# Kernel optimization log

Measured on AMD Instinct MI355X. Metric: run time of the kernel, lower is better.

Reference implementation:

```python
import jax, jax.numpy as jnp
import numpy as np

GROUPS = 8
HEADS = 8
EPS = 1e-5


def group_norm(x, w, b, groups=GROUPS, eps=EPS):
    # x: [B, C, D, H, W]
    B, C, D, H, W = x.shape
    xg = x.reshape(B, groups, C // groups, D, H, W)
    mu = xg.mean(axis=(2, 3, 4, 5), keepdims=True)
    var = xg.var(axis=(2, 3, 4, 5), keepdims=True)
    xn = ((xg - mu) / jnp.sqrt(var + eps)).reshape(B, C, D, H, W)
    return xn * w[None, :, None, None, None] + b[None, :, None, None, None]


def conv1x1(x, w, b):
    # 1x1x1 Conv3d == channel-mixing GEMM. w: [Cout, Cin], x: [B, Cin, D, H, W]
    y = jnp.einsum('oc,bcdhw->bodhw', w, x)
    return y + b[None, :, None, None, None]


def setup_inputs() -> dict:
    key = jax.random.key(0)
    ks = jax.random.split(key, 8)
    C, CTX = 512, 512
    B, D, H, W = 1, 16, 16, 16
    x = jax.random.normal(ks[0], (B, C, D, H, W), dtype=jnp.float32)
    context = jax.random.normal(ks[1], (B, CTX, D, H, W), dtype=jnp.float32)
    return {
        'x': x,
        'context': context,
        'norm_w': jnp.ones((C,), jnp.float32),
        'norm_b': jnp.zeros((C,), jnp.float32),
        'normc_w': jnp.ones((CTX,), jnp.float32),
        'normc_b': jnp.zeros((CTX,), jnp.float32),
        'q_w': jax.random.normal(ks[2], (C, C), jnp.float32) * 0.02,
        'q_b': jnp.zeros((C,), jnp.float32),
        'kv_w': jax.random.normal(ks[3], (2 * C, CTX), jnp.float32) * 0.02,
        'kv_b': jnp.zeros((2 * C,), jnp.float32),
        'proj_w': jax.random.normal(ks[4], (C, C), jnp.float32) * 0.02,
        'proj_b': jnp.zeros((C,), jnp.float32),
    }


def _split_heads(t, heads):
    # [B, (h c), D, H, W] -> [B, h, S, c] with S = D*H*W
    B, C, D, H, W = t.shape
    return t.reshape(B, heads, C // heads, D * H * W).transpose(0, 1, 3, 2)


def reference(x, context, norm_w, norm_b, normc_w, normc_b,
              q_w, q_b, kv_w, kv_b, proj_w, proj_b):
    B, C, D, H, W = x.shape
    h = group_norm(x, norm_w, norm_b)
    c = group_norm(context, normc_w, normc_b)
    q = conv1x1(h, q_w, q_b)
    kv = conv1x1(c, kv_w, kv_b)
    k, v = jnp.split(kv, 2, axis=1)
    q = _split_heads(q, HEADS)   # [B, h, S, c]
    k = _split_heads(k, HEADS)
    v = _split_heads(v, HEADS)
    scale = (C // HEADS) ** (-0.5)
    logits = jnp.einsum('bhqc,bhkc->bhqk', q, k) * scale
    attn = jax.nn.softmax(logits, axis=-1)
    out = jnp.einsum('bhqk,bhkc->bhqc', attn, v)
    # [B, h, S, c] -> [B, (h c), D, H, W]
    out = out.transpose(0, 1, 3, 2).reshape(B, C, D, H, W)
    out = conv1x1(out, proj_w, proj_b)
    return x + out
```

## Files before the change

kernel.cpp:

```cpp
#include <hip/hip_runtime.h>

typedef unsigned short u16;
typedef unsigned int u32;
typedef float f32x4 __attribute__((ext_vector_type(4)));
typedef __bf16 bf16x8 __attribute__((ext_vector_type(8)));
typedef u32 u32x4 __attribute__((ext_vector_type(4)));

#define LOG2E 1.44269504088896340736f

static __device__ __forceinline__ u16 f2bf(float f){ u32 u=__builtin_bit_cast(u32,f); u32 r=u+0x7fffu+((u>>16)&1u); return (u16)(r>>16); }
static __device__ __forceinline__ u32 pk2(float a,float b){ return (u32)f2bf(a)|((u32)f2bf(b)<<16); }
static __device__ __forceinline__ float fexp2(float x){
#if __has_builtin(__builtin_amdgcn_exp2f)
  return __builtin_amdgcn_exp2f(x);
#else
  float r; asm volatile("v_exp_f32 %0, %1" : "=v"(r) : "v"(x)); return r;
#endif
}
static __device__ __forceinline__ f32x4 mfma16(u32x4 a,u32x4 b,f32x4 c){
  return __builtin_amdgcn_mfma_f32_16x16x32_bf16(__builtin_bit_cast(bf16x8,a),__builtin_bit_cast(bf16x8,b),c,0,0,0);
}
static __device__ __forceinline__ u32x4 ldfrag(const u32* p){
  uint2 a=*(const uint2*)p; uint2 b=*(const uint2*)(p+2);
  u32x4 r; r.x=a.x; r.y=a.y; r.z=b.x; r.w=b.y; return r;
}
static __device__ __forceinline__ void stlds(u32* d, uint4 v){
  *(uint2*)d = make_uint2(v.x,v.y); *(uint2*)(d+2) = make_uint2(v.z,v.w);
}
static __device__ __forceinline__ uint4 pack8(float4 a,float4 b){
  uint4 o; o.x=pk2(a.x,a.y); o.y=pk2(a.z,a.w); o.z=pk2(b.x,b.y); o.w=pk2(b.z,b.w); return o;
}

__global__ __launch_bounds__(256) void k_stats(const float* __restrict__ x, const float* __restrict__ c,
                                               float* __restrict__ stats){
  const int g=blockIdx.x>>3, slice=blockIdx.x&7;
  const float* src=(g<8?x:c)+(size_t)(g&7)*262144+(size_t)slice*32768;
  const float4* p=(const float4*)src;
  const int t=threadIdx.x;
  float s1=0.f,s2=0.f;
  for(int i=0;i<32;i++){
    float4 v=p[t+i*256];
    s1+=v.x+v.y+v.z+v.w;
    s2+=v.x*v.x+v.y*v.y+v.z*v.z+v.w*v.w;
  }
  #pragma unroll
  for(int m=1;m<64;m<<=1){ s1+=__shfl_xor(s1,m,64); s2+=__shfl_xor(s2,m,64); }
  __shared__ float r1[4],r2[4];
  const int lane=t&63,w=t>>6;
  if(lane==0){ r1[w]=s1; r2[w]=s2; }
  __syncthreads();
  if(t==0){
    atomicAdd(&stats[2*g],   r1[0]+r1[1]+r1[2]+r1[3]);
    atomicAdd(&stats[2*g+1], r2[0]+r2[1]+r2[2]+r2[3]);
  }
}

__global__ __launch_bounds__(256) void k_prep(const float* __restrict__ qw,const float* __restrict__ qb,
    const float* __restrict__ kvw,const float* __restrict__ kvb,
    const float* __restrict__ nw,const float* __restrict__ nb,
    const float* __restrict__ ncw,const float* __restrict__ ncb,
    const float* __restrict__ pb,const float* __restrict__ stats,
    u16* __restrict__ Wall,float* __restrict__ biasAll){
  const int lane=threadIdx.x&63, w=threadIdx.x>>6;
  const int r=blockIdx.x*4+w;
  if(r>=1536){ if(lane==0) biasAll[r]=pb[r-1536]; return; }
  const bool isq = r<512;
  const float* Wsrc = isq ? qw+(size_t)r*512 : kvw+(size_t)(r-512)*512;
  const float* anw = isq ? nw : ncw;
  const float* anb = isq ? nb : ncb;
  const int gbase = isq ? 0 : 8;
  const float bin = isq ? qb[r] : kvb[r-512];
  const int ci0=lane*8;
  float4 wa=*(const float4*)(Wsrc+ci0);
  float4 wb=*(const float4*)(Wsrc+ci0+4);
  float wf[8]={wa.x,wa.y,wa.z,wa.w,wb.x,wb.y,wb.z,wb.w};
  float bp=0.f; u16 hb[8];
  #pragma unroll
  for(int j=0;j<8;j++){
    int ci=ci0+j;
    int g=gbase+(ci>>6);
    float mean=stats[2*g]*(1.f/262144.f);
    float var =stats[2*g+1]*(1.f/262144.f)-mean*mean;
    float rstd=rsqrtf(var+1e-5f);
    float alv=anw[ci]*rstd;
    float bev=anb[ci]-mean*alv;
    bp+=wf[j]*bev;
    hb[j]=f2bf(wf[j]*alv);
  }
  uint4 ov;
  ov.x=(u32)hb[0]|((u32)hb[1]<<16);
  ov.y=(u32)hb[2]|((u32)hb[3]<<16);
  ov.z=(u32)hb[4]|((u32)hb[5]<<16);
  ov.w=(u32)hb[6]|((u32)hb[7]<<16);
  *(uint4*)(Wall+(size_t)r*512+ci0)=ov;
  #pragma unroll
  for(int m=1;m<64;m<<=1) bp+=__shfl_xor(bp,m,64);
  if(lane==0) biasAll[r]=bin+bp;
}

template<int AMODE,int BMODE,int SMODE,int ZM>
__global__ __launch_bounds__(256) void k_gemm(const void* __restrict__ Av,const void* __restrict__ Av2,
    const void* __restrict__ Bv,const float* __restrict__ biasAll,const float* __restrict__ residf,
    void* __restrict__ out1,void* __restrict__ out2,float scale1,float scale2){
  __shared__ __align__(16) u32 As[2][64*18];
  __shared__ __align__(16) u32 Bs[2][128*18];
  const int t=threadIdx.x, lane=t&63, w=t>>6;
  const int wm=w&1, wn=w>>1, quad=lane>>4, l15=lane&15;
  const int m0=blockIdx.y*64, n0=blockIdx.x*128;
  const int z = ZM ? blockIdx.z : 0;
  const void* Aptr = (ZM && z) ? Av2 : Av;
  const u16* Bu = (const u16*)Bv + (BMODE==0 ? (size_t)z*512*512 : 0);
  const float* Bf = (const float*)Bv;
  const float* bias = biasAll + (ZM ? z*512 : 0);
  void* outv = (ZM && z) ? out2 : out1;
  const float scale = (ZM && z) ? scale2 : scale1;
  const int arow=t>>2, akc=(t&3)*8;
  const int cl=t>>3, s8=(t&7)*8;

  uint4 ra; float4 raf0, raf1;
  uint4 rb0, rb1; float4 rbf0, rbf1, rbf2, rbf3;

  auto loadAB=[&](int kk){
    if(AMODE==0){
      const u16* A=(const u16*)Aptr;
      ra=*(const uint4*)(A+(size_t)(m0+arow)*512+kk+akc);
    }else if(AMODE==1){
      const float* A=(const float*)Aptr;
      raf0=*(const float4*)(A+(size_t)(kk+cl)*4096+m0+s8);
      raf1=*(const float4*)(A+(size_t)(kk+cl)*4096+m0+s8+4);
    }else{
      const float* A=(const float*)Aptr;
      raf0=*(const float4*)(A+(size_t)(m0+arow)*512+kk+akc);
      raf1=*(const float4*)(A+(size_t)(m0+arow)*512+kk+akc+4);
    }
    if(BMODE==2){
      rbf0=*(const float4*)(Bf+(size_t)(kk+cl)*4096+n0+s8);
      rbf1=*(const float4*)(Bf+(size_t)(kk+cl)*4096+n0+s8+4);
      rbf2=*(const float4*)(Bf+(size_t)(kk+cl)*4096+n0+64+s8);
      rbf3=*(const float4*)(Bf+(size_t)(kk+cl)*4096+n0+64+s8+4);
    }else if(BMODE==1){
      rb0=*(const uint4*)(Bu+((size_t)((kk>>6)*4096+n0+arow))*64+(kk&63)+akc);
      rb1=*(const uint4*)(Bu+((size_t)((kk>>6)*4096+n0+64+arow))*64+(kk&63)+akc);
    }else{
      rb0=*(const uint4*)(Bu+(size_t)(n0+arow)*512+kk+akc);
      rb1=*(const uint4*)(Bu+(size_t)(n0+64+arow)*512+kk+akc);
    }
  };
  auto writeAB=[&](u32* Asb,u32* Bsb){
    if(AMODE==0){ stlds(&Asb[arow*18+(akc>>1)],ra); }
    else if(AMODE==1){
      float f[8]={raf0.x,raf0.y,raf0.z,raf0.w,raf1.x,raf1.y,raf1.z,raf1.w};
      u16* As16=(u16*)Asb;
      #pragma unroll
      for(int j=0;j<8;j++) As16[(s8+j)*36+cl]=f2bf(f[j]);
    }else{
      stlds(&Asb[arow*18+(akc>>1)],pack8(raf0,raf1));
    }
    if(BMODE==2){
      u16* Bs16=(u16*)Bsb;
      float f[8]={rbf0.x,rbf0.y,rbf0.z,rbf0.w,rbf1.x,rbf1.y,rbf1.z,rbf1.w};
      float g[8]={rbf2.x,rbf2.y,rbf2.z,rbf2.w,rbf3.x,rbf3.y,rbf3.z,rbf3.w};
      #pragma unroll
      for(int j=0;j<8;j++){
        Bs16[(s8+j)*36+cl]=f2bf(f[j]);
        Bs16[(64+s8+j)*36+cl]=f2bf(g[j]);
      }
    }else{
      stlds(&Bsb[arow*18+(akc>>1)],rb0);
      stlds(&Bsb[(64+arow)*18+(akc>>1)],rb1);
    }
  };

  f32x4 acc[2][4];
  #pragma unroll
  for(int i=0;i<2;i++)
    #pragma unroll
    for(int j=0;j<4;j++){ acc[i][j].x=0.f; acc[i][j].y=0.f; acc[i][j].z=0.f; acc[i][j].w=0.f; }

  auto compute=[&](const u32* Asb,const u32* Bsb){
    const u32* Ab=Asb+(wm*32+l15)*18+quad*4;
    const u32* Bb=Bsb+(wn*64+l15)*18+quad*4;
    u32x4 af[2], bfr[4];
    #pragma unroll
    for(int mt=0;mt<2;mt++) af[mt]=ldfrag(Ab+mt*288);
    #pragma unroll
    for(int nt=0;nt<4;nt++) bfr[nt]=ldfrag(Bb+nt*288);
    #pragma unroll
    for(int mt=0;mt<2;mt++)
      #pragma unroll
      for(int nt=0;nt<4;nt++) acc[mt][nt]=mfma16(af[mt],bfr[nt],acc[mt][nt]);
  };

  loadAB(0); writeAB(As[0],Bs[0]);
  __syncthreads();
  for(int kk=0;kk<512;kk+=64){
    loadAB(kk+32);
    compute(As[0],Bs[0]);
    writeAB(As[1],Bs[1]);
    __syncthreads();
    const bool n2=(kk+64)<512;
    if(n2) loadAB(kk+64);
    compute(As[1],Bs[1]);
    if(n2){ writeAB(As[0],Bs[0]); __syncthreads(); }
  }
  #pragma unroll
  for(int mt=0;mt<2;mt++)
    #pragma unroll
    for(int nt=0;nt<4;nt++){
      const int n = n0 + wn*64 + nt*16 + l15;
      if(SMODE==0){
        u16* out=(u16*)outv;
        const float bn = bias[n];
        const size_t base = ((size_t)((n>>6)*4096))*64 + (size_t)(n&63);
        #pragma unroll
        for(int r=0;r<4;r++){
          int m = m0 + wm*32 + mt*16 + quad*4 + r;
          out[base + (size_t)m*64] = f2bf((acc[mt][nt][r]+bn)*scale);
        }
      } else if(SMODE==1){
        u16* out=(u16*)outv;
        #pragma unroll
        for(int r=0;r<4;r++){
          int m = m0 + wm*32 + mt*16 + quad*4 + r;
          out[(size_t)m*4096+n] = f2bf(acc[mt][nt][r] + bias[m]);
        }
      } else {
        float* out=(float*)outv;
        #pragma unroll
        for(int r=0;r<4;r++){
          int m = m0 + wm*32 + mt*16 + quad*4 + r;
          out[(size_t)m*4096+n] = acc[mt][nt][r] + bias[m] + residf[(size_t)m*4096+n];
        }
      }
    }
}

__global__ __launch_bounds__(256) void k_attn(const u16* __restrict__ Qh,const u16* __restrict__ Kh,
                                              const u16* __restrict__ Vp,u16* __restrict__ Oh){
  __shared__ __align__(16) u32 Qs[64*34];
  __shared__ __align__(16) u32 Ks[2][64*34];
  __shared__ __align__(16) u32 Vs[2][64*34];
  __shared__ __align__(16) u32 Ps[4][16*34];
  const int t=threadIdx.x, lane=t&63, w=t>>6, quad=lane>>4, l15=lane&15;
  const int h=blockIdx.y, s0=blockIdx.x*64;
  const int srow=t>>2, sc=(t&3)*16;
  const u16* Kg = Kh + ((size_t)(h*4096+srow))*64 + sc;
  const u16* Vg = Vp + (size_t)(h*64+srow)*4096 + sc;
  { const u16* p = Qh + ((size_t)(h*4096+s0+srow))*64 + sc;
    stlds(&Qs[srow*34+(sc>>1)],   *(const uint4*)p);
    stlds(&Qs[srow*34+(sc>>1)+4], *(const uint4*)(p+8));
    stlds(&Ks[0][srow*34+(sc>>1)],   *(const uint4*)Kg);
    stlds(&Ks[0][srow*34+(sc>>1)+4], *(const uint4*)(Kg+8));
    stlds(&Vs[0][srow*34+(sc>>1)],   *(const uint4*)Vg);
    stlds(&Vs[0][srow*34+(sc>>1)+4], *(const uint4*)(Vg+8)); }
  __syncthreads();
  u32x4 qf[2];
  #pragma unroll
  for(int ks=0;ks<2;ks++) qf[ks]=ldfrag(&Qs[(w*16+l15)*34+ks*16+quad*4]);
  float lrun[4]; f32x4 oacc[4];
  #pragma unroll
  for(int r=0;r<4;r++) lrun[r]=0.f;
  #pragma unroll
  for(int nt=0;nt<4;nt++){ oacc[nt].x=0.f; oacc[nt].y=0.f; oacc[nt].z=0.f; oacc[nt].w=0.f; }

  u16* Pw=(u16*)Ps[w]+(quad*4)*68+l15;
  const u32* Pb=Ps[w]+l15*34+quad*4;

  auto halfstep=[&](const u32* Kc,const u32* Vc,u32* Kn,u32* Vn,int t0,bool pf){
    uint4 pk0,pk1,pv0,pv1;
    if(pf){
      const u16* kp=Kg+(size_t)(t0+64)*64;
      pk0=*(const uint4*)kp; pk1=*(const uint4*)(kp+8);
      const u16* vp=Vg+(t0+64);
      pv0=*(const uint4*)vp; pv1=*(const uint4*)(vp+8);
    }
    f32x4 sv[4];
    const u32* Kb=Kc+l15*34+quad*4;
    #pragma unroll
    for(int nt=0;nt<4;nt++){
      f32x4 zz; zz.x=0.f; zz.y=0.f; zz.z=0.f; zz.w=0.f;
      u32x4 k0=ldfrag(Kb+nt*544);
      u32x4 k1=ldfrag(Kb+nt*544+16);
      zz=mfma16(qf[0],k0,zz);
      sv[nt]=mfma16(qf[1],k1,zz);
    }
    #pragma unroll
    for(int nt=0;nt<4;nt++)
      #pragma unroll
      for(int r=0;r<4;r++){
        float p=fexp2(sv[nt][r]);
        sv[nt][r]=p;
        Pw[r*68+nt*16]=(u16)(__builtin_bit_cast(u32,p)>>16);
      }
    #pragma unroll
    for(int r=0;r<4;r++) lrun[r]+=(sv[0][r]+sv[1][r])+(sv[2][r]+sv[3][r]);
    const u32* Vb=Vc+l15*34+quad*4;
    #pragma unroll
    for(int ks=0;ks<2;ks++){
      u32x4 pfr=ldfrag(Pb+ks*16);
      #pragma unroll
      for(int nt=0;nt<4;nt++){
        u32x4 vf=ldfrag(Vb+nt*544+ks*16);
        oacc[nt]=mfma16(pfr,vf,oacc[nt]);
      }
    }
    if(pf){
      u32* Knw=Kn+srow*34+(sc>>1);
      u32* Vnw=Vn+srow*34+(sc>>1);
      stlds(Knw,pk0); stlds(Knw+4,pk1);
      stlds(Vnw,pv0); stlds(Vnw+4,pv1);
      __syncthreads();
    }
  };

  for(int t0=0;t0<4096;t0+=128){
    halfstep(Ks[0],Vs[0],Ks[1],Vs[1],t0,true);
    halfstep(Ks[1],Vs[1],Ks[0],Vs[0],t0+64,(t0+128)<4096);
  }

  #pragma unroll
  for(int r=0;r<4;r++){
    float l=lrun[r];
    #pragma unroll
    for(int m=1;m<16;m<<=1) l+=__shfl_xor(l,m,64);
    float inv=1.f/l;
    #pragma unroll
    for(int nt=0;nt<4;nt++) oacc[nt][r]*=inv;
  }
  #pragma unroll
  for(int nt=0;nt<4;nt++)
    #pragma unroll
    for(int r=0;r<4;r++)
      Oh[((size_t)(h*4096+s0+w*16+quad*4+r))*64 + nt*16 + l15]=f2bf(oacc[nt][r]);
}

extern "C" void kernel_launch(void* const* d_in, const int* in_sizes, int n_in,
                              void* d_out, int out_size, void* d_ws, size_t ws_size,
                              hipStream_t stream){
  (void)in_sizes; (void)n_in; (void)out_size; (void)ws_size;
  const float* x  =(const float*)d_in[0];
  const float* ctx=(const float*)d_in[1];
  const float* nw =(const float*)d_in[2];
  const float* nb =(const float*)d_in[3];
  const float* ncw=(const float*)d_in[4];
  const float* ncb=(const float*)d_in[5];
  const float* qw =(const float*)d_in[6];
  const float* qb =(const float*)d_in[7];
  const float* kvw=(const float*)d_in[8];
  const float* kvb=(const float*)d_in[9];
  const float* pw =(const float*)d_in[10];
  const float* pb =(const float*)d_in[11];
  float* out=(float*)d_out;
  char* ws=(char*)d_ws;
  float* stats  =(float*)ws;
  float* biasAll=(float*)(ws+256);
  u16* Wall=(u16*)(ws+16384);
  u16* Qh  =(u16*)(ws+1589248);
  u16* Kh  =(u16*)(ws+5783552);
  u16* Vp  =(u16*)(ws+9977856);
  u16* Oh  =(u16*)(ws+14172160);

  (void)hipMemsetAsync(stats,0,128,stream);
  k_stats<<<dim3(128),dim3(256),0,stream>>>(x,ctx,stats);
  k_prep<<<dim3(512),dim3(256),0,stream>>>(qw,qb,kvw,kvb,nw,nb,ncw,ncb,pb,stats,Wall,biasAll);
  k_gemm<1,0,0,1><<<dim3(4,64,2),dim3(256),0,stream>>>(x, ctx, Wall, biasAll, nullptr, Qh, Kh, 0.125f*LOG2E, 1.f);
  k_gemm<0,2,1,0><<<dim3(32,8),dim3(256),0,stream>>>(Wall+(size_t)1024*512, nullptr, ctx, biasAll+1024, nullptr, Vp, nullptr, 1.f, 1.f);
  k_attn<<<dim3(64,8),dim3(256),0,stream>>>(Qh,Kh,Vp,Oh);
  k_gemm<2,1,2,0><<<dim3(32,8),dim3(256),0,stream>>>(pw, nullptr, Oh, biasAll+1536, x, out, nullptr, 1.f, 1.f);
}
```

Baseline: 207.1 us.

## Split attention KV range across two wave groups and keep P in registers

The attention kernel now runs 512 threads per block. Two halves of four waves each process disjoint halves of the key/value sequence, and their partial outputs and row sums are merged through shared memory at the end. The S tile is computed transposed with 16x16x16 bf16 MFMAs, so the exponentiated probabilities can feed the PV MFMA directly from registers, which removes the per-wave P round-trip through LDS. This doubles parallelism for a grid of only 512 blocks. The cost is smaller MFMA shapes, an extra reduction step, and higher LDS and register pressure per block.

Result: faster. 189.7 us (-8.4%).

```diff
diff --git a/kernel.cpp b/kernel.cpp
--- a/kernel.cpp
+++ b/kernel.cpp
@@ -5,6 +5,8 @@
 typedef float f32x4 __attribute__((ext_vector_type(4)));
 typedef __bf16 bf16x8 __attribute__((ext_vector_type(8)));
 typedef u32 u32x4 __attribute__((ext_vector_type(4)));
+typedef u32 u32x2 __attribute__((ext_vector_type(2)));
+typedef short s16x4 __attribute__((ext_vector_type(4)));
 
 #define LOG2E 1.44269504088896340736f
 
@@ -20,9 +22,21 @@
 static __device__ __forceinline__ f32x4 mfma16(u32x4 a,u32x4 b,f32x4 c){
   return __builtin_amdgcn_mfma_f32_16x16x32_bf16(__builtin_bit_cast(bf16x8,a),__builtin_bit_cast(bf16x8,b),c,0,0,0);
 }
+#if __has_builtin(__builtin_amdgcn_mfma_f32_16x16x16bf16_1k)
+static __device__ __forceinline__ f32x4 mfma1k(s16x4 a,s16x4 b,f32x4 c){
+  return __builtin_amdgcn_mfma_f32_16x16x16bf16_1k(a,b,c,0,0,0);
+}
+#else
+static __device__ __forceinline__ f32x4 mfma1k(s16x4 a,s16x4 b,f32x4 c){
+  f32x4 d; asm("v_mfma_f32_16x16x16_bf16 %0, %1, %2, %3":"=v"(d):"v"(a),"v"(b),"v"(c)); return d;
+}
+#endif
 static __device__ __forceinline__ u32x4 ldfrag(const u32* p){
   uint2 a=*(const uint2*)p; uint2 b=*(const uint2*)(p+2);
   u32x4 r; r.x=a.x; r.y=a.y; r.z=b.x; r.w=b.y; return r;
+}
+static __device__ __forceinline__ s16x4 ld8(const u32* p){
+  return __builtin_bit_cast(s16x4, *(const u32x2*)p);
 }
 static __device__ __forceinline__ void stlds(u32* d, uint4 v){
   *(uint2*)d = make_uint2(v.x,v.y); *(uint2*)(d+2) = make_uint2(v.z,v.w);
@@ -235,103 +249,109 @@
     }
 }
 
-__global__ __launch_bounds__(256) void k_attn(const u16* __restrict__ Qh,const u16* __restrict__ Kh,
+__global__ __launch_bounds__(512,4) void k_attn(const u16* __restrict__ Qh,const u16* __restrict__ Kh,
                                               const u16* __restrict__ Vp,u16* __restrict__ Oh){
-  __shared__ __align__(16) u32 Qs[64*34];
-  __shared__ __align__(16) u32 Ks[2][64*34];
-  __shared__ __align__(16) u32 Vs[2][64*34];
-  __shared__ __align__(16) u32 Ps[4][16*34];
+  __shared__ __align__(16) u32 KS[2][2][64*34];
+  __shared__ __align__(16) u32 VS[2][2][64*34];
   const int t=threadIdx.x, lane=t&63, w=t>>6, quad=lane>>4, l15=lane&15;
+  const int half=w>>2, wq=w&3;
   const int h=blockIdx.y, s0=blockIdx.x*64;
-  const int srow=t>>2, sc=(t&3)*16;
-  const u16* Kg = Kh + ((size_t)(h*4096+srow))*64 + sc;
-  const u16* Vg = Vp + (size_t)(h*64+srow)*4096 + sc;
-  { const u16* p = Qh + ((size_t)(h*4096+s0+srow))*64 + sc;
-    stlds(&Qs[srow*34+(sc>>1)],   *(const uint4*)p);
-    stlds(&Qs[srow*34+(sc>>1)+4], *(const uint4*)(p+8));
-    stlds(&Ks[0][srow*34+(sc>>1)],   *(const uint4*)Kg);
-    stlds(&Ks[0][srow*34+(sc>>1)+4], *(const uint4*)(Kg+8));
-    stlds(&Vs[0][srow*34+(sc>>1)],   *(const uint4*)Vg);
-    stlds(&Vs[0][srow*34+(sc>>1)+4], *(const uint4*)(Vg+8)); }
-  __syncthreads();
-  u32x4 qf[2];
-  #pragma unroll
-  for(int ks=0;ks<2;ks++) qf[ks]=ldfrag(&Qs[(w*16+l15)*34+ks*16+quad*4]);
-  float lrun[4]; f32x4 oacc[4];
-  #pragma unroll
-  for(int r=0;r<4;r++) lrun[r]=0.f;
-  #pragma unroll
-  for(int nt=0;nt<4;nt++){ oacc[nt].x=0.f; oacc[nt].y=0.f; oacc[nt].z=0.f; oacc[nt].w=0.f; }
-
-  u16* Pw=(u16*)Ps[w]+(quad*4)*68+l15;
-  const u32* Pb=Ps[w]+l15*34+quad*4;
-
-  auto halfstep=[&](const u32* Kc,const u32* Vc,u32* Kn,u32* Vn,int t0,bool pf){
-    uint4 pk0,pk1,pv0,pv1;
-    if(pf){
-      const u16* kp=Kg+(size_t)(t0+64)*64;
-      pk0=*(const uint4*)kp; pk1=*(const uint4*)(kp+8);
-      const u16* vp=Vg+(t0+64);
-      pv0=*(const uint4*)vp; pv1=*(const uint4*)(vp+8);
-    }
+  const int tt=t&255, srow=tt>>2, sc=(tt&3)*16;
+  const u16* Kg = Kh + ((size_t)(h*4096 + half*2048 + srow))*64 + sc;
+  const u16* Vg = Vp + (size_t)(h*64+srow)*4096 + half*2048 + sc;
+  const u16* Qg = Qh + ((size_t)(h*4096+s0+wq*16+l15))*64;
+  s16x4 qf[4];
+  #pragma unroll
+  for(int kc=0;kc<4;kc++) qf[kc]=ld8((const u32*)(Qg + kc*16 + quad*4));
+
+  uint4 pk0,pk1,pv0,pv1;
+  auto loadKV=[&](int t0l){
+    const u16* kp=Kg+(size_t)t0l*64;
+    pk0=*(const uint4*)kp; pk1=*(const uint4*)(kp+8);
+    const u16* vp=Vg+t0l;
+    pv0=*(const uint4*)vp; pv1=*(const uint4*)(vp+8);
+  };
+  auto writeKV=[&](u32* Kb,u32* Vb){
+    u32* kw=Kb+srow*34+(sc>>1);
+    stlds(kw,pk0); stlds(kw+4,pk1);
+    u32* vw=Vb+srow*34+(sc>>1);
+    stlds(vw,pv0); stlds(vw+4,pv1);
+  };
+
+  float lrun=0.f; f32x4 oacc[4];
+  #pragma unroll
+  for(int cn=0;cn<4;cn++){ oacc[cn].x=0.f; oacc[cn].y=0.f; oacc[cn].z=0.f; oacc[cn].w=0.f; }
+
+  auto tilestep=[&](const u32* Kb,const u32* Vb){
     f32x4 sv[4];
-    const u32* Kb=Kc+l15*34+quad*4;
     #pragma unroll
     for(int nt=0;nt<4;nt++){
-      f32x4 zz; zz.x=0.f; zz.y=0.f; zz.z=0.f; zz.w=0.f;
-      u32x4 k0=ldfrag(Kb+nt*544);
-      u32x4 k1=ldfrag(Kb+nt*544+16);
-      zz=mfma16(qf[0],k0,zz);
-      sv[nt]=mfma16(qf[1],k1,zz);
-    }
-    #pragma unroll
-    for(int nt=0;nt<4;nt++)
-      #pragma unroll
-      for(int r=0;r<4;r++){
-        float p=fexp2(sv[nt][r]);
-        sv[nt][r]=p;
-        Pw[r*68+nt*16]=(u16)(__builtin_bit_cast(u32,p)>>16);
-      }
-    #pragma unroll
-    for(int r=0;r<4;r++) lrun[r]+=(sv[0][r]+sv[1][r])+(sv[2][r]+sv[3][r]);
-    const u32* Vb=Vc+l15*34+quad*4;
-    #pragma unroll
-    for(int ks=0;ks<2;ks++){
-      u32x4 pfr=ldfrag(Pb+ks*16);
-      #pragma unroll
-      for(int nt=0;nt<4;nt++){
-        u32x4 vf=ldfrag(Vb+nt*544+ks*16);
-        oacc[nt]=mfma16(pfr,vf,oacc[nt]);
-      }
-    }
-    if(pf){
-      u32* Knw=Kn+srow*34+(sc>>1);
-      u32* Vnw=Vn+srow*34+(sc>>1);
-      stlds(Knw,pk0); stlds(Knw+4,pk1);
-      stlds(Vnw,pv0); stlds(Vnw+4,pv1);
-      __syncthreads();
-    }
-  };
-
-  for(int t0=0;t0<4096;t0+=128){
-    halfstep(Ks[0],Vs[0],Ks[1],Vs[1],t0,true);
-    halfstep(Ks[1],Vs[1],Ks[0],Vs[0],t0+64,(t0+128)<4096);
-  }
-
-  #pragma unroll
-  for(int r=0;r<4;r++){
-    float l=lrun[r];
-    #pragma unroll
-    for(int m=1;m<16;m<<=1) l+=__shfl_xor(l,m,64);
-    float inv=1.f/l;
-    #pragma unroll
-    for(int nt=0;nt<4;nt++) oacc[nt][r]*=inv;
-  }
-  #pragma unroll
-  for(int nt=0;nt<4;nt++)
-    #pragma unroll
-    for(int r=0;r<4;r++)
-      Oh[((size_t)(h*4096+s0+w*16+quad*4+r))*64 + nt*16 + l15]=f2bf(oacc[nt][r]);
+      const u32* kb=Kb+(nt*16+l15)*34+quad*2;
+      f32x4 a; a.x=0.f; a.y=0.f; a.z=0.f; a.w=0.f;
+      #pragma unroll
+      for(int kc=0;kc<4;kc++) a=mfma1k(ld8(kb+kc*8),qf[kc],a);
+      sv[nt]=a;
+    }
+    s16x4 pfr[4];
+    #pragma unroll
+    for(int nt=0;nt<4;nt++){
+      float p0=fexp2(sv[nt].x),p1=fexp2(sv[nt].y),p2=fexp2(sv[nt].z),p3=fexp2(sv[nt].w);
+      lrun+=(p0+p1)+(p2+p3);
+      u32x2 pp;
+      pp.x=(__builtin_bit_cast(u32,p0)>>16)|(__builtin_bit_cast(u32,p1)&0xffff0000u);
+      pp.y=(__builtin_bit_cast(u32,p2)>>16)|(__builtin_bit_cast(u32,p3)&0xffff0000u);
+      pfr[nt]=__builtin_bit_cast(s16x4,pp);
+    }
+    #pragma unroll
+    for(int cn=0;cn<4;cn++){
+      const u32* vb=Vb+(cn*16+l15)*34+quad*2;
+      f32x4 a=oacc[cn];
+      #pragma unroll
+      for(int nt=0;nt<4;nt++) a=mfma1k(pfr[nt],ld8(vb+nt*8),a);
+      oacc[cn]=a;
+    }
+  };
+
+  loadKV(0); writeKV(KS[half][0],VS[half][0]);
+  __syncthreads();
+  for(int t0=0;t0<2048;t0+=128){
+    loadKV(t0+64);
+    tilestep(KS[half][0],VS[half][0]);
+    writeKV(KS[half][1],VS[half][1]);
+    __syncthreads();
+    const bool more=(t0+128)<2048;
+    if(more) loadKV(t0+128);
+    tilestep(KS[half][1],VS[half][1]);
+    if(more){ writeKV(KS[half][0],VS[half][0]); __syncthreads(); }
+  }
+  __syncthreads();
+  float* cb=(float*)KS[1];
+  const int cbi=(wq*64+lane)*17;
+  if(half==1){
+    #pragma unroll
+    for(int cn=0;cn<4;cn++)
+      #pragma unroll
+      for(int r=0;r<4;r++) cb[cbi+cn*4+r]=oacc[cn][r];
+    cb[cbi+16]=lrun;
+  }
+  __syncthreads();
+  if(half==0){
+    #pragma unroll
+    for(int cn=0;cn<4;cn++)
+      #pragma unroll
+      for(int r=0;r<4;r++) oacc[cn][r]+=cb[cbi+cn*4+r];
+    lrun+=cb[cbi+16];
+    float l=lrun;
+    l+=__shfl_xor(l,16,64);
+    l+=__shfl_xor(l,32,64);
+    #pragma unroll
+    for(int r=0;r<4;r++){
+      float inv=1.f/__shfl(l,quad*4+r,64);
+      #pragma unroll
+      for(int cn=0;cn<4;cn++)
+        Oh[((size_t)(h*4096+s0+wq*16+quad*4+r))*64 + cn*16 + l15]=f2bf(oacc[cn][r]*inv);
+    }
+  }
 }
 
 extern "C" void kernel_launch(void* const* d_in, const int* in_sizes, int n_in,
@@ -365,6 +385,6 @@
   k_prep<<<dim3(512),dim3(256),0,stream>>>(qw,qb,kvw,kvb,nw,nb,ncw,ncb,pb,stats,Wall,biasAll);
   k_gemm<1,0,0,1><<<dim3(4,64,2),dim3(256),0,stream>>>(x, ctx, Wall, biasAll, nullptr, Qh, Kh, 0.125f*LOG2E, 1.f);
   k_gemm<0,2,1,0><<<dim3(32,8),dim3(256),0,stream>>>(Wall+(size_t)1024*512, nullptr, ctx, biasAll+1024, nullptr, Vp, nullptr, 1.f, 1.f);
-  k_attn<<<dim3(64,8),dim3(256),0,stream>>>(Qh,Kh,Vp,Oh);
+  k_attn<<<dim3(64,8),dim3(512),0,stream>>>(Qh,Kh,Vp,Oh);
   k_gemm<2,1,2,0><<<dim3(32,8),dim3(256),0,stream>>>(pw, nullptr, Oh, biasAll+1536, x, out, nullptr, 1.f, 1.f);
 }
```
